# Kernel tuning notes

Measured on AMD Instinct MI355X. Metric: run time of the kernel, lower is better.

Reference implementation:

```python
import jax, jax.numpy as jnp
import numpy as np

H = 32          # hidden_dim (forced by targetLayer = Linear(4*32, 1))
IN = 1          # input_size per step
T = 129         # seq_len
S = 4           # 4 parallel LSTM streams: [main, f1, f2, f3]


def setup_inputs() -> dict:
    key = jax.random.key(0)
    ks = jax.random.split(key, 16)
    sc = 1.0 / np.sqrt(H)
    u = lambda k, shape: jax.random.uniform(k, shape, jnp.float32, -sc, sc)
    inp = {
        "x": jax.random.normal(ks[0], (S, T, IN), jnp.float32),
        # layer 0 (input -> hidden), stacked over the 4 LSTMs; gate order i,f,g,o
        "Wih0": u(ks[1], (S, 4 * H, IN)),
        "Whh0": u(ks[2], (S, 4 * H, H)),
        "bih0": u(ks[3], (S, 4 * H)),
        "bhh0": u(ks[4], (S, 4 * H)),
        # layer 1 (hidden -> hidden)
        "Wih1": u(ks[5], (S, 4 * H, H)),
        "Whh1": u(ks[6], (S, 4 * H, H)),
        "bih1": u(ks[7], (S, 4 * H)),
        "bhh1": u(ks[8], (S, 4 * H)),
        # output heads
        "Wt": u(ks[9], (1, 4 * H)),
        "bt": u(ks[10], (1,)),
        "Wf1": u(ks[11], (1, H)),
        "bf1": u(ks[12], (1,)),
        "Wf2": u(ks[13], (1, H)),
        "bf2": u(ks[14], (1,)),
    }
    return inp


def _cell(xin, h, c, Wih, Whh, bih, bhh):
    # xin: [S, in], h/c: [S, H]; fused 4-stream LSTM cell, PyTorch gate order i,f,g,o
    g = jnp.einsum('sgi,si->sg', Wih, xin) + jnp.einsum('sgh,sh->sg', Whh, h) + bih + bhh
    i, f, gg, o = jnp.split(g, 4, axis=-1)
    c2 = jax.nn.sigmoid(f) * c + jax.nn.sigmoid(i) * jnp.tanh(gg)
    h2 = jax.nn.sigmoid(o) * jnp.tanh(c2)
    return h2, c2


def reference(x, Wih0, Whh0, bih0, bhh0, Wih1, Whh1, bih1, bhh1, Wt, bt, Wf1, bf1, Wf2, bf2):
    z = jnp.zeros((S, H), x.dtype)

    def step(carry, xt):
        h0, c0, h1, c1 = carry
        h0, c0 = _cell(xt, h0, c0, Wih0, Whh0, bih0, bhh0)
        h1, c1 = _cell(h0, h1, c1, Wih1, Whh1, bih1, bhh1)
        return (h0, c0, h1, c1), None

    xs = jnp.transpose(x, (1, 0, 2))  # [T, S, IN]
    (h0, c0, h1, c1), _ = jax.lax.scan(step, (z, z, z, z), xs)
    hlast = h1  # [S, H], last-step top-layer output; order: main, f1, f2, f3

    targetIn = hlast.reshape(1, S * H)          # torch.cat(...).view(-1, 4H)
    targetOut = targetIn @ Wt.T + bt            # [1, 1]
    f1Out = (hlast[1:2] @ Wf1.T + bf1).reshape(1, 1, 1)
    f2Out = (hlast[2:3] @ Wf2.T + bf2).reshape(1, 1, 1)
    f3Out = (hlast[3:4] @ Wf2.T + bf2).reshape(1, 1, 1)  # original bug: reuses featureLayer2
    return (targetOut, f1Out, f2Out, f3Out)
```

## Files before the change

kernel.cpp:

```cpp
#include <hip/hip_runtime.h>


#define HDIM 32
#define SEQT 129
#define NS 4

__device__ __forceinline__ float fsig(float x) {
  return 1.0f / (1.0f + __expf(-x));
}
__device__ __forceinline__ float swap_hi(float v) {
  auto r = __builtin_amdgcn_permlane32_swap(__float_as_int(v), __float_as_int(v),
                                            false, false);
  return __int_as_float(r[1]);
}
#define PINF(w) asm volatile("" : "+v"(w))

__global__ __launch_bounds__(256) __attribute__((amdgpu_waves_per_eu(1, 1)))
void lstm4_kernel(const float* __restrict__ x,
                  const float* __restrict__ Wih0, const float* __restrict__ Whh0,
                  const float* __restrict__ bih0, const float* __restrict__ bhh0,
                  const float* __restrict__ Wih1, const float* __restrict__ Whh1,
                  const float* __restrict__ bih1, const float* __restrict__ bhh1,
                  const float* __restrict__ Wt,  const float* __restrict__ bt,
                  const float* __restrict__ Wf1, const float* __restrict__ bf1,
                  const float* __restrict__ Wf2, const float* __restrict__ bf2,
                  float* __restrict__ out) {
  const int tid = threadIdx.x;
  const int s = tid >> 6;
  const int l = tid & 63;

  __shared__ float xs[NS * SEQT + 1];
  __shared__ __align__(16) float hb0[NS][HDIM];
  __shared__ __align__(16) float hb1[NS][HDIM];

  for (int i = tid; i < NS * SEQT; i += 256) xs[i] = x[i];
  if (tid == 0) xs[NS * SEQT] = 0.0f;
  for (int i = tid; i < NS * HDIM; i += 256) {
    (&hb0[0][0])[i] = 0.0f;
    (&hb1[0][0])[i] = 0.0f;
  }
  __syncthreads();

  const int r1 = s * 128 + l;
  const int r2 = s * 128 + l + 64;

  float wh0a[HDIM], wh0b[HDIM], wi1a[HDIM], wi1b[HDIM], wh1a[HDIM], wh1b[HDIM];
  #pragma unroll
  for (int j = 0; j < 8; ++j) {
    float4 v;
    v = *(const float4*)(Whh0 + r1 * 32 + 4 * j);
    wh0a[4*j] = v.x; wh0a[4*j+1] = v.y; wh0a[4*j+2] = v.z; wh0a[4*j+3] = v.w;
    v = *(const float4*)(Whh0 + r2 * 32 + 4 * j);
    wh0b[4*j] = v.x; wh0b[4*j+1] = v.y; wh0b[4*j+2] = v.z; wh0b[4*j+3] = v.w;
    v = *(const float4*)(Wih1 + r1 * 32 + 4 * j);
    wi1a[4*j] = v.x; wi1a[4*j+1] = v.y; wi1a[4*j+2] = v.z; wi1a[4*j+3] = v.w;
    v = *(const float4*)(Wih1 + r2 * 32 + 4 * j);
    wi1b[4*j] = v.x; wi1b[4*j+1] = v.y; wi1b[4*j+2] = v.z; wi1b[4*j+3] = v.w;
    v = *(const float4*)(Whh1 + r1 * 32 + 4 * j);
    wh1a[4*j] = v.x; wh1a[4*j+1] = v.y; wh1a[4*j+2] = v.z; wh1a[4*j+3] = v.w;
    v = *(const float4*)(Whh1 + r2 * 32 + 4 * j);
    wh1b[4*j] = v.x; wh1b[4*j+1] = v.y; wh1b[4*j+2] = v.z; wh1b[4*j+3] = v.w;
  }
  #pragma unroll
  for (int k = 0; k < HDIM; ++k) {
    PINF(wh0a[k]); PINF(wh0b[k]);
    PINF(wi1a[k]); PINF(wi1b[k]);
    PINF(wh1a[k]); PINF(wh1b[k]);
  }
  const float wx0a = Wih0[r1];
  const float wx0b = Wih0[r2];
  const float b0a  = bih0[r1] + bhh0[r1];
  const float b0b  = bih0[r2] + bhh0[r2];
  const float b1a  = bih1[r1] + bhh1[r1];
  const float b1b  = bih1[r2] + bhh1[r2];

  const bool  lo   = (l < 32);
  const float m2   = lo ? 2.0f : 1.0f;
  const float add2 = lo ? -1.0f : 0.0f;

  float c0 = 0.0f, c1 = 0.0f;
  float h1new = 0.0f;

  float hv[HDIM];
  #pragma unroll
  for (int k = 0; k < HDIM; ++k) hv[k] = 0.0f;

  float xt = xs[s * SEQT];

  #pragma unroll 1
  for (int t = 0; t < SEQT; ++t) {
    const float xt_next = xs[s * SEQT + t + 1];

    float gv[HDIM];
    #pragma unroll
    for (int j = 0; j < 8; ++j) {
      const float4 g4 = *(const float4*)&hb1[s][4 * j];
      gv[4*j] = g4.x; gv[4*j+1] = g4.y; gv[4*j+2] = g4.z; gv[4*j+3] = g4.w;
    }

    float p1a = b0a, p1b = 0.f, p1c = 0.f, p1d = 0.f;
    float p2a = b0b, p2b = 0.f, p2c = 0.f, p2d = 0.f;
    p1a = fmaf(wx0a, xt, p1a);
    p2a = fmaf(wx0b, xt, p2a);
    #pragma unroll
    for (int j = 0; j < 8; ++j) {
      p1a = fmaf(wh0a[4*j+0], hv[4*j+0], p1a);
      p1b = fmaf(wh0a[4*j+1], hv[4*j+1], p1b);
      p1c = fmaf(wh0a[4*j+2], hv[4*j+2], p1c);
      p1d = fmaf(wh0a[4*j+3], hv[4*j+3], p1d);
      p2a = fmaf(wh0b[4*j+0], hv[4*j+0], p2a);
      p2b = fmaf(wh0b[4*j+1], hv[4*j+1], p2b);
      p2c = fmaf(wh0b[4*j+2], hv[4*j+2], p2c);
      p2d = fmaf(wh0b[4*j+3], hv[4*j+3], p2d);
    }
    const float v1 = (p1a + p1b) + (p1c + p1d);
    const float v2 = (p2a + p2b) + (p2c + p2d);

    const float a1  = fsig(v1);
    const float sv2 = fsig(v2 * m2);
    const float a2  = fmaf(sv2, m2, add2);
    const float p   = a1 * a2;
    const float swf = swap_hi(a1);
    const float swo = swap_hi(a2);
    c0 = fmaf(swf, c0, p);
    const float th0 = fmaf(fsig(2.0f * c0), 2.0f, -1.0f);
    const float h0new = swo * th0;

    if (lo) hb0[s][l] = h0new;

    float hv2[HDIM];
    #pragma unroll
    for (int j = 0; j < 8; ++j) {
      const float4 h4 = *(const float4*)&hb0[s][4 * j];
      hv2[4*j] = h4.x; hv2[4*j+1] = h4.y; hv2[4*j+2] = h4.z; hv2[4*j+3] = h4.w;
    }

    float q1a = b1a, q1b = 0.f, q1c = 0.f, q1d = 0.f;
    float q2a = b1b, q2b = 0.f, q2c = 0.f, q2d = 0.f;
    #pragma unroll
    for (int j = 0; j < 8; ++j) {
      q1a = fmaf(wh1a[4*j+0], gv[4*j+0], q1a);
      q1b = fmaf(wh1a[4*j+1], gv[4*j+1], q1b);
      q1c = fmaf(wh1a[4*j+2], gv[4*j+2], q1c);
      q1d = fmaf(wh1a[4*j+3], gv[4*j+3], q1d);
      q2a = fmaf(wh1b[4*j+0], gv[4*j+0], q2a);
      q2b = fmaf(wh1b[4*j+1], gv[4*j+1], q2b);
      q2c = fmaf(wh1b[4*j+2], gv[4*j+2], q2c);
      q2d = fmaf(wh1b[4*j+3], gv[4*j+3], q2d);
    }
    #pragma unroll
    for (int j = 0; j < 8; ++j) {
      q1a = fmaf(wi1a[4*j+0], hv2[4*j+0], q1a);
      q1b = fmaf(wi1a[4*j+1], hv2[4*j+1], q1b);
      q1c = fmaf(wi1a[4*j+2], hv2[4*j+2], q1c);
      q1d = fmaf(wi1a[4*j+3], hv2[4*j+3], q1d);
      q2a = fmaf(wi1b[4*j+0], hv2[4*j+0], q2a);
      q2b = fmaf(wi1b[4*j+1], hv2[4*j+1], q2b);
      q2c = fmaf(wi1b[4*j+2], hv2[4*j+2], q2c);
      q2d = fmaf(wi1b[4*j+3], hv2[4*j+3], q2d);
    }
    const float w1 = (q1a + q1b) + (q1c + q1d);
    const float w2 = (q2a + q2b) + (q2c + q2d);

    const float A1  = fsig(w1);
    const float sw2 = fsig(w2 * m2);
    const float A2  = fmaf(sw2, m2, add2);
    const float P   = A1 * A2;
    const float SWF = swap_hi(A1);
    const float SWO = swap_hi(A2);
    c1 = fmaf(SWF, c1, P);
    const float th1 = fmaf(fsig(2.0f * c1), 2.0f, -1.0f);
    h1new = SWO * th1;

    if (lo) hb1[s][l] = h1new;

    #pragma unroll
    for (int k = 0; k < HDIM; ++k) hv[k] = hv2[k];

    xt = xt_next;
  }

  __syncthreads();

  float acc = 0.0f;
  if (s == 0) {
    acc = fmaf(Wt[l], (&hb1[0][0])[l], Wt[l + 64] * (&hb1[0][0])[l + 64]);
  } else {
    const float* Wf = (s == 1) ? Wf1 : Wf2;
    if (l < HDIM) acc = Wf[l] * hb1[s][l];
  }
  #pragma unroll
  for (int off = 32; off > 0; off >>= 1) acc += __shfl_xor(acc, off);
  if (l == 0) {
    const float bias = (s == 0) ? bt[0] : ((s == 1) ? bf1[0] : bf2[0]);
    out[s] = acc + bias;
  }
}

extern "C" void kernel_launch(void* const* d_in, const int* in_sizes, int n_in,
                              void* d_out, int out_size, void* d_ws, size_t ws_size,
                              hipStream_t stream) {
  const float* x    = (const float*)d_in[0];
  const float* Wih0 = (const float*)d_in[1];
  const float* Whh0 = (const float*)d_in[2];
  const float* bih0 = (const float*)d_in[3];
  const float* bhh0 = (const float*)d_in[4];
  const float* Wih1 = (const float*)d_in[5];
  const float* Whh1 = (const float*)d_in[6];
  const float* bih1 = (const float*)d_in[7];
  const float* bhh1 = (const float*)d_in[8];
  const float* Wt   = (const float*)d_in[9];
  const float* bt   = (const float*)d_in[10];
  const float* Wf1  = (const float*)d_in[11];
  const float* bf1  = (const float*)d_in[12];
  const float* Wf2  = (const float*)d_in[13];
  const float* bf2  = (const float*)d_in[14];
  float* out = (float*)d_out;

  lstm4_kernel<<<1, 256, 0, stream>>>(x, Wih0, Whh0, bih0, bhh0,
                                      Wih1, Whh1, bih1, bhh1,
                                      Wt, bt, Wf1, bf1, Wf2, bf2, out);
}
```

Measured before the change: 180.9 us.

## Hoist layer-1 recurrent dot ahead of layer-0 activation and widen accumulators

Computes the layer-1 Whh·h1 partial dot product right after the layer-0 dot, before the layer-0 gate nonlinearity and the LDS round trip. This moves independent work off the critical path between the two layers. The dot product now uses 8 accumulators instead of 4 for more instruction-level parallelism. The sigmoid uses a hardware reciprocal, and the register-pinning asm and waves_per_eu attribute are removed, which may change register allocation.

Measured after the change: 177.5 us. No clear change (-1.9%).

```diff
diff --git a/kernel.cpp b/kernel.cpp
--- a/kernel.cpp
+++ b/kernel.cpp
@@ -6,16 +6,33 @@
 #define NS 4
 
 __device__ __forceinline__ float fsig(float x) {
-  return 1.0f / (1.0f + __expf(-x));
+  return __builtin_amdgcn_rcpf(1.0f + __expf(-x));
 }
 __device__ __forceinline__ float swap_hi(float v) {
   auto r = __builtin_amdgcn_permlane32_swap(__float_as_int(v), __float_as_int(v),
                                             false, false);
   return __int_as_float(r[1]);
 }
-#define PINF(w) asm volatile("" : "+v"(w))
 
-__global__ __launch_bounds__(256) __attribute__((amdgpu_waves_per_eu(1, 1)))
+__device__ __forceinline__ float dot32(const float* __restrict__ w,
+                                       const float* __restrict__ h, float seed) {
+  float a0 = seed, a1 = 0.f, a2 = 0.f, a3 = 0.f;
+  float a4 = 0.f, a5 = 0.f, a6 = 0.f, a7 = 0.f;
+  #pragma unroll
+  for (int j = 0; j < 4; ++j) {
+    a0 = fmaf(w[8*j+0], h[8*j+0], a0);
+    a1 = fmaf(w[8*j+1], h[8*j+1], a1);
+    a2 = fmaf(w[8*j+2], h[8*j+2], a2);
+    a3 = fmaf(w[8*j+3], h[8*j+3], a3);
+    a4 = fmaf(w[8*j+4], h[8*j+4], a4);
+    a5 = fmaf(w[8*j+5], h[8*j+5], a5);
+    a6 = fmaf(w[8*j+6], h[8*j+6], a6);
+    a7 = fmaf(w[8*j+7], h[8*j+7], a7);
+  }
+  return ((a0 + a1) + (a2 + a3)) + ((a4 + a5) + (a6 + a7));
+}
+
+__global__ __launch_bounds__(256)
 void lstm4_kernel(const float* __restrict__ x,
                   const float* __restrict__ Wih0, const float* __restrict__ Whh0,
                   const float* __restrict__ bih0, const float* __restrict__ bhh0,
@@ -61,12 +78,6 @@
     v = *(const float4*)(Whh1 + r2 * 32 + 4 * j);
     wh1b[4*j] = v.x; wh1b[4*j+1] = v.y; wh1b[4*j+2] = v.z; wh1b[4*j+3] = v.w;
   }
-  #pragma unroll
-  for (int k = 0; k < HDIM; ++k) {
-    PINF(wh0a[k]); PINF(wh0b[k]);
-    PINF(wi1a[k]); PINF(wi1b[k]);
-    PINF(wh1a[k]); PINF(wh1b[k]);
-  }
   const float wx0a = Wih0[r1];
   const float wx0b = Wih0[r2];
   const float b0a  = bih0[r1] + bhh0[r1];
@@ -98,23 +109,11 @@
       gv[4*j] = g4.x; gv[4*j+1] = g4.y; gv[4*j+2] = g4.z; gv[4*j+3] = g4.w;
     }
 
-    float p1a = b0a, p1b = 0.f, p1c = 0.f, p1d = 0.f;
-    float p2a = b0b, p2b = 0.f, p2c = 0.f, p2d = 0.f;
-    p1a = fmaf(wx0a, xt, p1a);
-    p2a = fmaf(wx0b, xt, p2a);
-    #pragma unroll
-    for (int j = 0; j < 8; ++j) {
-      p1a = fmaf(wh0a[4*j+0], hv[4*j+0], p1a);
-      p1b = fmaf(wh0a[4*j+1], hv[4*j+1], p1b);
-      p1c = fmaf(wh0a[4*j+2], hv[4*j+2], p1c);
-      p1d = fmaf(wh0a[4*j+3], hv[4*j+3], p1d);
-      p2a = fmaf(wh0b[4*j+0], hv[4*j+0], p2a);
-      p2b = fmaf(wh0b[4*j+1], hv[4*j+1], p2b);
-      p2c = fmaf(wh0b[4*j+2], hv[4*j+2], p2c);
-      p2d = fmaf(wh0b[4*j+3], hv[4*j+3], p2d);
-    }
-    const float v1 = (p1a + p1b) + (p1c + p1d);
-    const float v2 = (p2a + p2b) + (p2c + p2d);
+    const float v1 = dot32(wh0a, hv, fmaf(wx0a, xt, b0a));
+    const float v2 = dot32(wh0b, hv, fmaf(wx0b, xt, b0b));
+
+    const float e1 = dot32(wh1a, gv, b1a);
+    const float e2 = dot32(wh1b, gv, b1b);
 
     const float a1  = fsig(v1);
     const float sv2 = fsig(v2 * m2);
@@ -135,32 +134,8 @@
       hv2[4*j] = h4.x; hv2[4*j+1] = h4.y; hv2[4*j+2] = h4.z; hv2[4*j+3] = h4.w;
     }
 
-    float q1a = b1a, q1b = 0.f, q1c = 0.f, q1d = 0.f;
-    float q2a = b1b, q2b = 0.f, q2c = 0.f, q2d = 0.f;
-    #pragma unroll
-    for (int j = 0; j < 8; ++j) {
-      q1a = fmaf(wh1a[4*j+0], gv[4*j+0], q1a);
-      q1b = fmaf(wh1a[4*j+1], gv[4*j+1], q1b);
-      q1c = fmaf(wh1a[4*j+2], gv[4*j+2], q1c);
-      q1d = fmaf(wh1a[4*j+3], gv[4*j+3], q1d);
-      q2a = fmaf(wh1b[4*j+0], gv[4*j+0], q2a);
-      q2b = fmaf(wh1b[4*j+1], gv[4*j+1], q2b);
-      q2c = fmaf(wh1b[4*j+2], gv[4*j+2], q2c);
-      q2d = fmaf(wh1b[4*j+3], gv[4*j+3], q2d);
-    }
-    #pragma unroll
-    for (int j = 0; j < 8; ++j) {
-      q1a = fmaf(wi1a[4*j+0], hv2[4*j+0], q1a);
-      q1b = fmaf(wi1a[4*j+1], hv2[4*j+1], q1b);
-      q1c = fmaf(wi1a[4*j+2], hv2[4*j+2], q1c);
-      q1d = fmaf(wi1a[4*j+3], hv2[4*j+3], q1d);
-      q2a = fmaf(wi1b[4*j+0], hv2[4*j+0], q2a);
-      q2b = fmaf(wi1b[4*j+1], hv2[4*j+1], q2b);
-      q2c = fmaf(wi1b[4*j+2], hv2[4*j+2], q2c);
-      q2d = fmaf(wi1b[4*j+3], hv2[4*j+3], q2d);
-    }
-    const float w1 = (q1a + q1b) + (q1c + q1d);
-    const float w2 = (q2a + q2b) + (q2c + q2d);
+    const float w1 = dot32(wi1a, hv2, e1);
+    const float w2 = dot32(wi1b, hv2, e2);
 
     const float A1  = fsig(w1);
     const float sw2 = fsig(w2 * m2);
```
